# Optimization experiments

Measured on AMD Instinct MI355X. Metric: run time of the kernel, lower is better.

Reference implementation:

```python
import jax, jax.numpy as jnp
import numpy as np

D_MODEL = 1024
N_HEADS = 16
HEAD_DIM = D_MODEL // N_HEADS
B, T = 4, 2048
EPS = 1e-5


def _layernorm(x, w, b):
    mu = jnp.mean(x, axis=-1, keepdims=True)
    var = jnp.mean(jnp.square(x - mu), axis=-1, keepdims=True)
    return (x - mu) * jax.lax.rsqrt(var + EPS) * w + b


def _heads(x, w, b):
    # x: [B,T,D]; w stored [in,out] so y = x @ w + b (== torch Linear)
    y = x @ w + b
    return y.reshape(B, T, N_HEADS, HEAD_DIM).transpose(0, 2, 1, 3)  # [B,H,T,hd]


def _attention(q, k, v):
    scores = jnp.einsum('bhqd,bhkd->bhqk', q, k) / np.sqrt(HEAD_DIM).astype(np.float32)
    attn = jax.nn.softmax(scores, axis=-1)  # dropout is identity in eval mode
    o = jnp.einsum('bhqk,bhkd->bhqd', attn, v)
    return o.transpose(0, 2, 1, 3).reshape(B, T, D_MODEL)


def setup_inputs() -> dict:
    key = jax.random.key(0)
    ks = jax.random.split(key, 16)
    s = 1.0 / np.sqrt(D_MODEL)
    def lin(k, din, dout):
        kw, kb = jax.random.split(k)
        return (jax.random.uniform(kw, (din, dout), jnp.float32, -s, s),
                jax.random.uniform(kb, (dout,), jnp.float32, -s, s))
    inp = {}
    inp['temporal_tokens'] = jax.random.normal(ks[0], (B, T, D_MODEL), jnp.float32)
    inp['feature_tokens'] = jax.random.normal(ks[1], (B, T, D_MODEL), jnp.float32)
    names = ['qt', 'kf', 'vf', 'qf', 'kt', 'vt', 'ot', 'of']
    for i, n in enumerate(names):
        w, b = lin(ks[2 + i], D_MODEL, D_MODEL)
        inp[n + '_w'], inp[n + '_b'] = w, b
    inp['fus1_w'], inp['fus1_b'] = lin(ks[10], 2 * D_MODEL, D_MODEL)
    inp['fus2_w'], inp['fus2_b'] = lin(ks[11], D_MODEL, D_MODEL)
    for n in ['ln_fus', 'ln_t', 'ln_f']:
        inp[n + '_w'] = jnp.ones((D_MODEL,), jnp.float32)
        inp[n + '_b'] = jnp.zeros((D_MODEL,), jnp.float32)
    return inp


def reference(temporal_tokens, feature_tokens,
              qt_w, qt_b, kf_w, kf_b, vf_w, vf_b,
              qf_w, qf_b, kt_w, kt_b, vt_w, vt_b,
              ot_w, ot_b, of_w, of_b,
              fus1_w, fus1_b, fus2_w, fus2_b,
              ln_fus_w, ln_fus_b, ln_t_w, ln_t_b, ln_f_w, ln_f_b):
    # temporal -> feature cross attention
    Qt = _heads(temporal_tokens, qt_w, qt_b)
    Kf = _heads(feature_tokens, kf_w, kf_b)
    Vf = _heads(feature_tokens, vf_w, vf_b)
    attn_t = _attention(Qt, Kf, Vf) @ ot_w + ot_b
    fused_t = _layernorm(temporal_tokens + attn_t, ln_t_w, ln_t_b)
    # feature -> temporal cross attention
    Qf = _heads(feature_tokens, qf_w, qf_b)
    Kt = _heads(temporal_tokens, kt_w, kt_b)
    Vt = _heads(temporal_tokens, vt_w, vt_b)
    attn_f = _attention(Qf, Kt, Vt) @ of_w + of_b
    fused_f = _layernorm(feature_tokens + attn_f, ln_f_w, ln_f_b)
    # fusion MLP
    combined = jnp.concatenate([fused_t, fused_f], axis=-1)  # [B,T,2D]
    h = jax.nn.gelu(combined @ fus1_w + fus1_b, approximate=False)
    fused = _layernorm(h @ fus2_w + fus2_b, ln_fus_w, ln_fus_b)
    return fused
```

## Files before the change

### kernel.cpp

```cpp
#include <hip/hip_runtime.h>
#include <math.h>

typedef __attribute__((ext_vector_type(8))) short short8;
typedef __attribute__((ext_vector_type(4))) short short4v;
typedef __attribute__((ext_vector_type(4))) float floatx4;
typedef __attribute__((ext_vector_type(16))) float floatx16;

#define GLOBAL_AS __attribute__((address_space(1)))
#define LDS_AS __attribute__((address_space(3)))

__device__ __forceinline__ float bf2f(unsigned short u) {
    unsigned int x = ((unsigned int)u) << 16;
    return __builtin_bit_cast(float, x);
}
__device__ __forceinline__ unsigned short f2bf(float f) {
    unsigned int u = __builtin_bit_cast(unsigned int, f);
    u += 0x7fffu + ((u >> 16) & 1u);
    return (unsigned short)(u >> 16);
}

struct WX {
    const float* src[10];
    unsigned long long dst[10];
    int r64[10];
    int cum[11];
};

__global__ __launch_bounds__(256) void prep_kernel(
    WX P, unsigned short* __restrict__ base,
    const float* __restrict__ ta, const float* __restrict__ tb,
    unsigned short* __restrict__ oa, unsigned short* __restrict__ ob)
{
    __shared__ unsigned short T[64][72];
    const int bx = blockIdx.x;
    if (bx >= P.cum[10]) {
        const int cb = bx - P.cum[10];
        const float* in = cb < 1024 ? ta : tb;
        unsigned short* out = cb < 1024 ? oa : ob;
        const size_t b0 = (size_t)(cb & 1023) * 8192;
        #pragma unroll
        for (int j = 0; j < 8; ++j) {
            const size_t i = b0 + (size_t)j * 1024 + threadIdx.x * 4;
            float4 f = *(const float4*)(in + i);
            unsigned short o[4] = {f2bf(f.x), f2bf(f.y), f2bf(f.z), f2bf(f.w)};
            *(uint2*)(out + i) = *(const uint2*)o;
        }
        return;
    }
    int w = 0;
    #pragma unroll
    for (int i = 0; i < 10; ++i) if (bx >= P.cum[i + 1]) w = i + 1;
    const int tix = bx - P.cum[w];
    const int R = P.r64[w] * 64;
    const int r0 = (tix >> 4) * 64, c0 = (tix & 15) * 64;
    const float* in = P.src[w];
    unsigned short* out = base + P.dst[w];
    const int t = threadIdx.x;
    {
        const int r = t >> 2, cc = (t & 3) * 16;
        const float* p = in + (size_t)(r0 + r) * 1024 + c0 + cc;
        #pragma unroll
        for (int j = 0; j < 16; j += 4) {
            float4 f = *(const float4*)(p + j);
            T[cc + j + 0][r] = f2bf(f.x);
            T[cc + j + 1][r] = f2bf(f.y);
            T[cc + j + 2][r] = f2bf(f.z);
            T[cc + j + 3][r] = f2bf(f.w);
        }
    }
    __syncthreads();
    {
        const int c = t >> 2, rr = (t & 3) * 16;
        unsigned short* q = out + (size_t)(c0 + c) * R + r0 + rr;
        *(uint4*)(q)     = *(const uint4*)(&T[c][rr]);
        *(uint4*)(q + 8) = *(const uint4*)(&T[c][rr + 8]);
    }
}

#define GEMM_CORE(A_, B_, Kdim)                                               \
    const int tid = threadIdx.x;                                              \
    const int wave = tid >> 6, lane = tid & 63;                               \
    const int l32 = lane & 31, hi = lane >> 5;                                \
    const int wm = (wave & 1) * 64, wn = (wave >> 1) * 64;                    \
    const int srow8 = lane >> 3, c8 = lane & 7;                               \
    const int scol = (c8 ^ srow8) * 8;                                        \
    floatx16 acc[2][2];                                                       \
    _Pragma("unroll")                                                         \
    for (int i = 0; i < 2; ++i)                                               \
        _Pragma("unroll")                                                     \
        for (int j = 0; j < 2; ++j)                                           \
            _Pragma("unroll")                                                 \
            for (int r = 0; r < 16; ++r) acc[i][j][r] = 0.f;                  \
    const unsigned short* pa[4];                                              \
    const unsigned short* pb[4];                                              \
    _Pragma("unroll")                                                         \
    for (int i = 0; i < 4; ++i) {                                             \
        pa[i] = (A_) + (size_t)(bm + i * 32 + wave * 8 + srow8) * (Kdim) + scol; \
        pb[i] = (B_) + (size_t)(bn + i * 32 + wave * 8 + srow8) * (Kdim) + scol; \
    }                                                                         \
    int aoff[2][4], boff[2][4];                                               \
    _Pragma("unroll")                                                         \
    for (int f = 0; f < 2; ++f)                                               \
        _Pragma("unroll")                                                     \
        for (int s = 0; s < 4; ++s) {                                         \
            const int cg = ((s * 2 + hi) ^ (l32 & 7)) * 8;                    \
            aoff[f][s] = (wm + f * 32 + l32) * 64 + cg;                       \
            boff[f][s] = (wn + f * 32 + l32) * 64 + cg;                       \
        }                                                                     \
    for (int k0 = 0; k0 < (Kdim); k0 += 64) {                                 \
        _Pragma("unroll")                                                     \
        for (int i = 0; i < 4; ++i) {                                         \
            __builtin_amdgcn_global_load_lds((const GLOBAL_AS void*)(pa[i] + k0), \
                (LDS_AS void*)(As + i * 2048 + wave * 512), 16, 0, 0);        \
            __builtin_amdgcn_global_load_lds((const GLOBAL_AS void*)(pb[i] + k0), \
                (LDS_AS void*)(Bs + i * 2048 + wave * 512), 16, 0, 0);        \
        }                                                                     \
        __syncthreads();                                                      \
        _Pragma("unroll")                                                     \
        for (int s = 0; s < 4; ++s) {                                         \
            short8 af[2], bf[2];                                              \
            _Pragma("unroll")                                                 \
            for (int f = 0; f < 2; ++f) {                                     \
                af[f] = *(const short8*)&As[aoff[f][s]];                      \
                bf[f] = *(const short8*)&Bs[boff[f][s]];                      \
            }                                                                 \
            _Pragma("unroll")                                                 \
            for (int mi = 0; mi < 2; ++mi)                                    \
                _Pragma("unroll")                                             \
                for (int ni = 0; ni < 2; ++ni)                                \
                    acc[mi][ni] = __builtin_amdgcn_mfma_f32_32x32x16_bf16(    \
                        bf[ni], af[mi], acc[mi][ni], 0, 0, 0);                \
        }                                                                     \
        __syncthreads();                                                      \
    }

template <int MODE>
__global__ __launch_bounds__(256) void gemm_kernel(
    const unsigned short* __restrict__ A,
    const unsigned short* __restrict__ Wt,
    const float* __restrict__ bias,
    unsigned short* __restrict__ C,
    int N, int K)
{
    __shared__ unsigned short As[128 * 64];
    __shared__ unsigned short Bs[128 * 64];
    const int bm = blockIdx.x * 128, bn = blockIdx.y * 128;
    GEMM_CORE(A, Wt, K)

    #pragma unroll
    for (int mi = 0; mi < 2; ++mi) {
        const int m = bm + wm + mi * 32 + l32;
        #pragma unroll
        for (int ni = 0; ni < 2; ++ni) {
            #pragma unroll
            for (int rg = 0; rg < 4; ++rg) {
                const int n0 = bn + wn + ni * 32 + rg * 8 + hi * 4;
                float4 bv = *(const float4*)&bias[n0];
                float v[4];
                #pragma unroll
                for (int r = 0; r < 4; ++r)
                    v[r] = acc[mi][ni][rg * 4 + r] + ((const float*)&bv)[r];
                if (MODE == 2) {
                    #pragma unroll
                    for (int r = 0; r < 4; ++r)
                        v[r] = 0.5f * v[r] * (1.0f + erff(v[r] * 0.70710678118f));
                }
                unsigned short o[4] = {f2bf(v[0]), f2bf(v[1]), f2bf(v[2]), f2bf(v[3])};
                *(uint2*)&C[(size_t)m * N + n0] = *(const uint2*)o;
            }
        }
    }
}

__global__ __launch_bounds__(256) void gemm_out_kernel(
    const unsigned short* __restrict__ A0, const unsigned short* __restrict__ W0,
    const float* __restrict__ bi0, const float* __restrict__ r0, unsigned short* __restrict__ C0,
    const unsigned short* __restrict__ A1, const unsigned short* __restrict__ W1,
    const float* __restrict__ bi1, const float* __restrict__ r1, unsigned short* __restrict__ C1)
{
    __shared__ unsigned short As[128 * 64];
    __shared__ unsigned short Bs[128 * 64];
    const int s1 = blockIdx.y >> 3;
    const unsigned short* A = s1 ? A1 : A0;
    const unsigned short* Wt = s1 ? W1 : W0;
    const float* bias = s1 ? bi1 : bi0;
    const float* resid = s1 ? r1 : r0;
    unsigned short* C = s1 ? C1 : C0;
    const int bm = blockIdx.x * 128, bn = (blockIdx.y & 7) * 128;
    GEMM_CORE(A, Wt, 1024)

    #pragma unroll
    for (int mi = 0; mi < 2; ++mi) {
        const int m = bm + wm + mi * 32 + l32;
        #pragma unroll
        for (int ni = 0; ni < 2; ++ni) {
            #pragma unroll
            for (int rg = 0; rg < 4; ++rg) {
                const int n0 = bn + wn + ni * 32 + rg * 8 + hi * 4;
                float4 bv = *(const float4*)&bias[n0];
                float4 rv = *(const float4*)&resid[(size_t)m * 1024 + n0];
                float v[4];
                v[0] = acc[mi][ni][rg * 4 + 0] + bv.x + rv.x;
                v[1] = acc[mi][ni][rg * 4 + 1] + bv.y + rv.y;
                v[2] = acc[mi][ni][rg * 4 + 2] + bv.z + rv.z;
                v[3] = acc[mi][ni][rg * 4 + 3] + bv.w + rv.w;
                unsigned short o[4] = {f2bf(v[0]), f2bf(v[1]), f2bf(v[2]), f2bf(v[3])};
                *(uint2*)&C[(size_t)m * 1024 + n0] = *(const uint2*)o;
            }
        }
    }
}

__global__ __launch_bounds__(256) void gemm_qkv_kernel(
    const unsigned short* __restrict__ At, const unsigned short* __restrict__ Wt3t,
    const float* __restrict__ tb0, const float* __restrict__ tb1, const float* __restrict__ tb2,
    unsigned short* __restrict__ to0, unsigned short* __restrict__ to1, unsigned short* __restrict__ to2,
    const unsigned short* __restrict__ Af, const unsigned short* __restrict__ Wt3f,
    const float* __restrict__ fb0, const float* __restrict__ fb1, const float* __restrict__ fb2,
    unsigned short* __restrict__ fo0, unsigned short* __restrict__ fo1, unsigned short* __restrict__ fo2,
    float scale0)
{
    __shared__ unsigned short As[128 * 64];
    __shared__ unsigned short Bs[128 * 64];
    const int str = blockIdx.y >= 24;
    const unsigned short* A = str ? Af : At;
    const unsigned short* Wt = str ? Wt3f : Wt3t;
    const int byy = str ? (blockIdx.y - 24) : blockIdx.y;
    const int buf = byy >> 3;
    const int bn = byy * 128;
    const int cn = (byy & 7) * 128;
    const float* bias = str ? (buf == 0 ? fb0 : (buf == 1 ? fb1 : fb2))
                            : (buf == 0 ? tb0 : (buf == 1 ? tb1 : tb2));
    unsigned short* C = str ? (buf == 0 ? fo0 : (buf == 1 ? fo1 : fo2))
                            : (buf == 0 ? to0 : (buf == 1 ? to1 : to2));
    const float scale = buf == 0 ? scale0 : 1.0f;
    const int bm = blockIdx.x * 128;
    GEMM_CORE(A, Wt, 1024)

    #pragma unroll
    for (int mi = 0; mi < 2; ++mi) {
        const int m = bm + wm + mi * 32 + l32;
        #pragma unroll
        for (int ni = 0; ni < 2; ++ni) {
            #pragma unroll
            for (int rg = 0; rg < 4; ++rg) {
                const int n0 = cn + wn + ni * 32 + rg * 8 + hi * 4;
                float4 bv = *(const float4*)&bias[n0];
                unsigned short o[4];
                #pragma unroll
                for (int r = 0; r < 4; ++r)
                    o[r] = f2bf((acc[mi][ni][rg * 4 + r] + ((const float*)&bv)[r]) * scale);
                if (buf == 2) {
                    const int b = m >> 11, t = m & 2047;
                    const int h = n0 >> 6, d0 = n0 & 63;
                    const int tsw = t ^ ((d0 & 8) ? 4 : 0);
                    unsigned short* vb = C + ((size_t)(b * 16 + h) * 64) * 2048 + tsw;
                    #pragma unroll
                    for (int r = 0; r < 4; ++r) vb[(size_t)(d0 + r) * 2048] = o[r];
                } else {
                    *(uint2*)&C[(size_t)m * 1024 + n0] = *(const uint2*)o;
                }
            }
        }
    }
}

__global__ __launch_bounds__(256) void flash_kernel(
    const unsigned short* __restrict__ Q0, const unsigned short* __restrict__ K0,
    const unsigned short* __restrict__ V0, unsigned short* __restrict__ O0,
    const unsigned short* __restrict__ Q1, const unsigned short* __restrict__ K1,
    const unsigned short* __restrict__ V1, unsigned short* __restrict__ O1)
{
    __shared__ unsigned short Ks[64 * 64];
    __shared__ unsigned short Vs[64 * 64];

    const int bid = blockIdx.x;
    const int p = (bid & 7) * 16 + (bid >> 7);
    const int qt = (bid >> 3) & 15;
    const int s1 = p >= 64;
    const int rem = p & 63;
    const int b = rem >> 4, h = rem & 15;
    const unsigned short* Q = s1 ? Q1 : Q0;
    const unsigned short* Kmat = s1 ? K1 : K0;
    const unsigned short* Vtp = s1 ? V1 : V0;
    unsigned short* O = s1 ? O1 : O0;
    const int q0 = qt * 128;

    const int tid = threadIdx.x;
    const int wave = tid >> 6, lane = tid & 63;
    const int quad = lane >> 4, l16 = lane & 15;

    const unsigned short* qp = Q + (size_t)(b * 2048 + q0 + wave * 32 + l16) * 1024 + h * 64;
    short8 qf[2][2];
    qf[0][0] = *(const short8*)(qp + quad * 8);
    qf[0][1] = *(const short8*)(qp + 32 + quad * 8);
    qf[1][0] = *(const short8*)(qp + 16 * 1024 + quad * 8);
    qf[1][1] = *(const short8*)(qp + 16 * 1024 + 32 + quad * 8);

    const int srow8 = lane >> 3;
    const int c8 = lane & 7;
    const int rit0 = wave * 16 + srow8;
    const int rit1 = rit0 + 8;
    const int col0 = (c8 ^ (rit0 & 7)) * 8;
    const int col1 = (c8 ^ (rit1 & 7)) * 8;
    const unsigned short* kbase = Kmat + (size_t)b * 2048 * 1024 + h * 64;
    const unsigned short* vbase = Vtp + (size_t)(b * 16 + h) * 64 * 2048;
    unsigned short* lk0 = Ks + (wave * 16) * 64;
    unsigned short* lk1 = lk0 + 8 * 64;
    unsigned short* lv0 = Vs + (wave * 16) * 64;
    unsigned short* lv1 = lv0 + 8 * 64;

    int koff[4][2];
    #pragma unroll
    for (int nt = 0; nt < 4; ++nt)
        #pragma unroll
        for (int hh = 0; hh < 2; ++hh)
            koff[nt][hh] = (nt * 16 + l16) * 64 + (((hh * 4 + quad) ^ (l16 & 7)) * 8);
    int voff[4][4];
    #pragma unroll
    for (int dt = 0; dt < 4; ++dt)
        #pragma unroll
        for (int nt = 0; nt < 4; ++nt)
            voff[dt][nt] = (dt * 16 + l16) * 64 +
                           (((nt * 2 + (quad >> 1)) ^ (l16 & 7)) * 8) +
                           (((quad & 1) ^ (l16 >> 3)) * 4);

    floatx4 oa[2][4], la[2];
    #pragma unroll
    for (int qg = 0; qg < 2; ++qg) {
        la[qg] = (floatx4){0.f, 0.f, 0.f, 0.f};
        #pragma unroll
        for (int dt = 0; dt < 4; ++dt) oa[qg][dt] = (floatx4){0.f, 0.f, 0.f, 0.f};
    }
    const short4v vone = {(short)0x3F80, (short)0x3F80, (short)0x3F80, (short)0x3F80};

    for (int kt = 0; kt < 32; ++kt) {
        const unsigned short* kg0 = kbase + (size_t)(kt * 64 + rit0) * 1024 + col0;
        const unsigned short* kg1 = kbase + (size_t)(kt * 64 + rit1) * 1024 + col1;
        const unsigned short* vg0 = vbase + (size_t)rit0 * 2048 + kt * 64 + col0;
        const unsigned short* vg1 = vbase + (size_t)rit1 * 2048 + kt * 64 + col1;
        __builtin_amdgcn_global_load_lds((const GLOBAL_AS void*)kg0, (LDS_AS void*)lk0, 16, 0, 0);
        __builtin_amdgcn_global_load_lds((const GLOBAL_AS void*)kg1, (LDS_AS void*)lk1, 16, 0, 0);
        __builtin_amdgcn_global_load_lds((const GLOBAL_AS void*)vg0, (LDS_AS void*)lv0, 16, 0, 0);
        __builtin_amdgcn_global_load_lds((const GLOBAL_AS void*)vg1, (LDS_AS void*)lv1, 16, 0, 0);
        __syncthreads();

        short4v pf[2][4];
        #pragma unroll
        for (int nt = 0; nt < 4; ++nt) {
            short8 k0 = *(const short8*)&Ks[koff[nt][0]];
            short8 k1 = *(const short8*)&Ks[koff[nt][1]];
            #pragma unroll
            for (int qg = 0; qg < 2; ++qg) {
                floatx4 s = (floatx4){0.f, 0.f, 0.f, 0.f};
                s = __builtin_amdgcn_mfma_f32_16x16x32_bf16(k0, qf[qg][0], s, 0, 0, 0);
                s = __builtin_amdgcn_mfma_f32_16x16x32_bf16(k1, qf[qg][1], s, 0, 0, 0);
                float p0 = __builtin_amdgcn_exp2f(s[0]);
                float p1 = __builtin_amdgcn_exp2f(s[1]);
                float p2 = __builtin_amdgcn_exp2f(s[2]);
                float p3 = __builtin_amdgcn_exp2f(s[3]);
                union { unsigned u[2]; short4v s4; } pk;
                asm("v_cvt_pk_bf16_f32 %0, %1, %2"
                    : "=v"(pk.u[0]) : "v"(p0), "v"(p1));
                asm("v_cvt_pk_bf16_f32 %0, %1, %2"
                    : "=v"(pk.u[1]) : "v"(p2), "v"(p3));
                pf[qg][nt] = pk.s4;
                la[qg] = __builtin_amdgcn_mfma_f32_16x16x16bf16_1k(vone, pf[qg][nt], la[qg], 0, 0, 0);
            }
        }
        #pragma unroll
        for (int dt = 0; dt < 4; ++dt)
            #pragma unroll
            for (int nt = 0; nt < 4; ++nt) {
                short4v vf = *(const short4v*)&Vs[voff[dt][nt]];
                oa[0][dt] = __builtin_amdgcn_mfma_f32_16x16x16bf16_1k(vf, pf[0][nt], oa[0][dt], 0, 0, 0);
                oa[1][dt] = __builtin_amdgcn_mfma_f32_16x16x16bf16_1k(vf, pf[1][nt], oa[1][dt], 0, 0, 0);
            }
        __syncthreads();
    }

    #pragma unroll
    for (int qg = 0; qg < 2; ++qg) {
        const float linv = 1.0f / la[qg][0];
        unsigned short* orow = O + (size_t)(b * 2048 + q0 + wave * 32 + qg * 16 + l16) * 1024 + h * 64;
        #pragma unroll
        for (int dt = 0; dt < 4; ++dt) {
            unsigned short ob[4];
            #pragma unroll
            for (int r = 0; r < 4; ++r) ob[r] = f2bf(oa[qg][dt][r] * linv);
            *(uint2*)(orow + dt * 16 + quad * 4) = *(const uint2*)ob;
        }
    }
}

__global__ __launch_bounds__(256) void ln2_kernel(
    const unsigned short* __restrict__ in0, const unsigned short* __restrict__ in1,
    unsigned short* __restrict__ out,
    const float* __restrict__ w0, const float* __restrict__ b0,
    const float* __restrict__ w1, const float* __restrict__ b1)
{
    __shared__ float red[8];
    const int sel = blockIdx.x >> 13;
    const int row = blockIdx.x & 8191;
    const unsigned short* in = sel ? in1 : in0;
    const float* w = sel ? w1 : w0;
    const float* bb = sel ? b1 : b0;
    const int tid = threadIdx.x;
    const int wave = tid >> 6, lane = tid & 63;
    uint2 raw = *(const uint2*)(in + (size_t)row * 1024 + tid * 4);
    float v[4];
    v[0] = bf2f((unsigned short)(raw.x & 0xffffu));
    v[1] = bf2f((unsigned short)(raw.x >> 16));
    v[2] = bf2f((unsigned short)(raw.y & 0xffffu));
    v[3] = bf2f((unsigned short)(raw.y >> 16));
    float s = v[0] + v[1] + v[2] + v[3];
    float sq = v[0] * v[0] + v[1] * v[1] + v[2] * v[2] + v[3] * v[3];
    #pragma unroll
    for (int m = 1; m < 64; m <<= 1) { s += __shfl_xor(s, m); sq += __shfl_xor(sq, m); }
    if (lane == 0) { red[wave] = s; red[4 + wave] = sq; }
    __syncthreads();
    s = red[0] + red[1] + red[2] + red[3];
    sq = red[4] + red[5] + red[6] + red[7];
    const float mu = s * (1.0f / 1024.0f);
    const float var = sq * (1.0f / 1024.0f) - mu * mu;
    const float rstd = rsqrtf(var + 1e-5f);
    unsigned short ob[4];
    #pragma unroll
    for (int j = 0; j < 4; ++j)
        ob[j] = f2bf((v[j] - mu) * rstd * w[tid * 4 + j] + bb[tid * 4 + j]);
    *(uint2*)(out + (size_t)row * 2048 + sel * 1024 + tid * 4) = *(uint2*)ob;
}

__global__ __launch_bounds__(256) void ln_final_kernel(
    const unsigned short* __restrict__ in, float* __restrict__ out,
    const float* __restrict__ w, const float* __restrict__ bias)
{
    __shared__ float red[8];
    const int row = blockIdx.x;
    const int tid = threadIdx.x;
    const int wave = tid >> 6, lane = tid & 63;
    uint2 raw = *(const uint2*)(in + (size_t)row * 1024 + tid * 4);
    float v[4];
    v[0] = bf2f((unsigned short)(raw.x & 0xffffu));
    v[1] = bf2f((unsigned short)(raw.x >> 16));
    v[2] = bf2f((unsigned short)(raw.y & 0xffffu));
    v[3] = bf2f((unsigned short)(raw.y >> 16));
    float s = v[0] + v[1] + v[2] + v[3];
    float sq = v[0] * v[0] + v[1] * v[1] + v[2] * v[2] + v[3] * v[3];
    #pragma unroll
    for (int m = 1; m < 64; m <<= 1) { s += __shfl_xor(s, m); sq += __shfl_xor(sq, m); }
    if (lane == 0) { red[wave] = s; red[4 + wave] = sq; }
    __syncthreads();
    s = red[0] + red[1] + red[2] + red[3];
    sq = red[4] + red[5] + red[6] + red[7];
    const float mu = s * (1.0f / 1024.0f);
    const float var = sq * (1.0f / 1024.0f) - mu * mu;
    const float rstd = rsqrtf(var + 1e-5f);
    float o[4];
    #pragma unroll
    for (int j = 0; j < 4; ++j)
        o[j] = (v[j] - mu) * rstd * w[tid * 4 + j] + bias[tid * 4 + j];
    *(float4*)(out + (size_t)row * 1024 + tid * 4) = (float4){o[0], o[1], o[2], o[3]};
}

extern "C" void kernel_launch(void* const* d_in, const int* in_sizes, int n_in,
                              void* d_out, int out_size, void* d_ws, size_t ws_size,
                              hipStream_t stream)
{
    (void)in_sizes; (void)n_in; (void)out_size; (void)ws_size;
    const float* temporal = (const float*)d_in[0];
    const float* feature  = (const float*)d_in[1];
    const float* qt_w = (const float*)d_in[2];
    const float* qt_b = (const float*)d_in[3];
    const float* kf_w = (const float*)d_in[4];
    const float* kf_b = (const float*)d_in[5];
    const float* vf_w = (const float*)d_in[6];
    const float* vf_b = (const float*)d_in[7];
    const float* qf_w = (const float*)d_in[8];
    const float* qf_b = (const float*)d_in[9];
    const float* kt_w = (const float*)d_in[10];
    const float* kt_b = (const float*)d_in[11];
    const float* vt_w = (const float*)d_in[12];
    const float* vt_b = (const float*)d_in[13];
    const float* ot_w = (const float*)d_in[14];
    const float* ot_b = (const float*)d_in[15];
    const float* of_w = (const float*)d_in[16];
    const float* of_b = (const float*)d_in[17];
    const float* fus1_w = (const float*)d_in[18];
    const float* fus1_b = (const float*)d_in[19];
    const float* fus2_w = (const float*)d_in[20];
    const float* fus2_b = (const float*)d_in[21];
    const float* ln_fus_w = (const float*)d_in[22];
    const float* ln_fus_b = (const float*)d_in[23];
    const float* ln_t_w = (const float*)d_in[24];
    const float* ln_t_b = (const float*)d_in[25];
    const float* ln_f_w = (const float*)d_in[26];
    const float* ln_f_b = (const float*)d_in[27];

    unsigned short* p = (unsigned short*)d_ws;
    const size_t EW = 1024ull * 1024;
    const size_t ET = 8192ull * 1024;
    unsigned short* WT3t = p;
    unsigned short* WT3f = p + 3 * EW;
    unsigned short* WTot = p + 6 * EW;
    unsigned short* WTof = p + 7 * EW;
    unsigned short* WTf1 = p + 8 * EW;
    unsigned short* WTf2 = p + 10 * EW;
    size_t off = 11 * EW;
    unsigned short* Tb = p + off; off += ET;
    unsigned short* Fb = p + off; off += ET;
    unsigned short* Qt = p + off; off += ET;
    unsigned short* Kt = p + off; off += ET;
    unsigned short* Vt = p + off; off += ET;
    unsigned short* Qf = p + off; off += ET;
    unsigned short* Kf = p + off; off += ET;
    unsigned short* Vf = p + off; off += ET;
    unsigned short* VfT = p + off; off += ET;
    unsigned short* VtT = p + off; off += ET;
    unsigned short* attnT = p + off; off += ET;
    unsigned short* attnF = p + off; off += ET;
    unsigned short* yT = Qt;
    unsigned short* yF = Qf;
    unsigned short* comb = Kt;
    unsigned short* hbuf = Kf;
    unsigned short* y2 = Vf;
    (void)Vt;

    const float SC = 0.125f * 1.4426950408889634f;

    {
        WX P;
        const float* srcs[10] = {qt_w, kt_w, vt_w, qf_w, kf_w, vf_w,
                                 ot_w, of_w, fus1_w, fus2_w};
        unsigned long long dsts[10] = {
            0, EW, 2 * EW,
            3 * EW, 4 * EW, 5 * EW,
            6 * EW, 7 * EW, 8 * EW, 10 * EW};
        int cum = 0;
        P.cum[0] = 0;
        for (int i = 0; i < 10; ++i) {
            P.src[i] = srcs[i];
            P.dst[i] = dsts[i];
            P.r64[i] = (i == 8) ? 32 : 16;
            cum += P.r64[i] * 16;
            P.cum[i + 1] = cum;
        }
        prep_kernel<<<cum + 2048, 256, 0, stream>>>(P, p, temporal, feature, Tb, Fb);
    }

    const dim3 gb(256);
    gemm_qkv_kernel<<<dim3(64, 48), gb, 0, stream>>>(
        Tb, WT3t, qt_b, kt_b, vt_b, Qt, Kt, VtT,
        Fb, WT3f, qf_b, kf_b, vf_b, Qf, Kf, VfT, SC);
    flash_kernel<<<2048, gb, 0, stream>>>(
        Qt, Kf, VfT, attnT, Qf, Kt, VtT, attnF);
    gemm_out_kernel<<<dim3(64, 16), gb, 0, stream>>>(
        attnT, WTot, ot_b, temporal, yT,
        attnF, WTof, of_b, feature,  yF);
    ln2_kernel<<<16384, gb, 0, stream>>>(yT, yF, comb, ln_t_w, ln_t_b, ln_f_w, ln_f_b);
    gemm_kernel<2><<<dim3(64, 8), gb, 0, stream>>>(comb, WTf1, fus1_b, hbuf, 1024, 2048);
    gemm_kernel<0><<<dim3(64, 8), gb, 0, stream>>>(hbuf, WTf2, fus2_b, y2, 1024, 1024);
    ln_final_kernel<<<8192, gb, 0, stream>>>(y2, (float*)d_out, ln_fus_w, ln_fus_b);
}
```

Before: 676.1 us.

## Rewrite GEMM core as 256x256 tiles with double-buffered LDS pipeline

Replaces the 128x128 single-buffer GEMM core with a 256x256 tile computed by 8 waves using 16x16x32 MFMAs. Global-to-LDS loads are double-buffered and interleaved with the MFMA phases, using explicit vmcnt waits, barriers and setprio. All four GEMM kernels and their launch grids are adapted. The aim is to hide load latency and get more reuse per tile. The cost is a 128KB LDS footprint and heavy register use, and the grids shrink to as few as 128 blocks for the fusion GEMMs, which may underfill the GPU.

```diff
diff --git a/kernel.cpp b/kernel.cpp
--- a/kernel.cpp
+++ b/kernel.cpp
@@ -77,141 +77,200 @@
     }
 }
 
-#define GEMM_CORE(A_, B_, Kdim)                                               \
+#define G256_DECL(A_, B_, Kdim)                                               \
     const int tid = threadIdx.x;                                              \
     const int wave = tid >> 6, lane = tid & 63;                               \
-    const int l32 = lane & 31, hi = lane >> 5;                                \
-    const int wm = (wave & 1) * 64, wn = (wave >> 1) * 64;                    \
-    const int srow8 = lane >> 3, c8 = lane & 7;                               \
-    const int scol = (c8 ^ srow8) * 8;                                        \
-    floatx16 acc[2][2];                                                       \
+    const int quad = lane >> 4, l16 = lane & 15;                              \
+    const int wr = wave >> 2, wc = wave & 3;                                  \
+    const int lrow8 = lane >> 3, lc8 = lane & 7;                              \
+    floatx4 acc[8][4];                                                        \
     _Pragma("unroll")                                                         \
-    for (int i = 0; i < 2; ++i)                                               \
+    for (int i = 0; i < 8; ++i)                                               \
         _Pragma("unroll")                                                     \
-        for (int j = 0; j < 2; ++j)                                           \
+        for (int j = 0; j < 4; ++j) acc[i][j] = (floatx4){0.f, 0.f, 0.f, 0.f}; \
+    const unsigned short* sA[4];                                              \
+    const unsigned short* sB[4];                                              \
+    int ldst[4];                                                              \
+    _Pragma("unroll")                                                         \
+    for (int h = 0; h < 2; ++h)                                               \
+        _Pragma("unroll")                                                     \
+        for (int j = 0; j < 2; ++j) {                                         \
+            const int r0 = h * 128 + j * 64 + wave * 8;                       \
+            const int r = r0 + lrow8;                                         \
+            const int cg = lc8 ^ (r & 7);                                     \
+            sA[h * 2 + j] = (A_) + (size_t)(bm + r) * (Kdim) + cg * 8;        \
+            sB[h * 2 + j] = (B_) + (size_t)(bn + r) * (Kdim) + cg * 8;        \
+            ldst[h * 2 + j] = r0 * 64;                                        \
+        }
+
+#define G256_STG_A(s_) __builtin_amdgcn_global_load_lds(                      \
+    (const GLOBAL_AS void*)(sA[s_] + ko), (LDS_AS void*)(L + cb + ldst[s_]), 16, 0, 0)
+#define G256_STG_B(s_) __builtin_amdgcn_global_load_lds(                      \
+    (const GLOBAL_AS void*)(sB[s_] + ko), (LDS_AS void*)(L + cb + 16384 + ldst[s_]), 16, 0, 0)
+
+#define G256_LDA(mh_)                                                         \
+    _Pragma("unroll")                                                         \
+    for (int mi = 0; mi < 4; ++mi) {                                          \
+        const int r = (mh_) * 128 + wr * 64 + mi * 16 + l16;                  \
+        _Pragma("unroll")                                                     \
+        for (int kk = 0; kk < 2; ++kk)                                        \
+            afc[mi][kk] = *(const short8*)&L[cb + r * 64 +                    \
+                (((kk * 4 + quad) ^ (r & 7)) * 8)];                           \
+    }
+#define G256_LDB(nh_)                                                         \
+    _Pragma("unroll")                                                         \
+    for (int nj = 0; nj < 2; ++nj) {                                          \
+        const int r = (nh_) * 128 + wc * 32 + nj * 16 + l16;                  \
+        _Pragma("unroll")                                                     \
+        for (int kk = 0; kk < 2; ++kk)                                        \
+            bfr[(nh_) * 2 + nj][kk] = *(const short8*)&L[cb + 16384 + r * 64 +\
+                (((kk * 4 + quad) ^ (r & 7)) * 8)];                           \
+    }
+
+#define G256_FENCE() do {                                                     \
+    asm volatile("s_waitcnt lgkmcnt(0)" ::: "memory");                        \
+    __builtin_amdgcn_sched_barrier(0);                                        \
+    __builtin_amdgcn_s_barrier(); } while (0)
+
+#define G256_MM(mh_, nb_) do {                                                \
+    __builtin_amdgcn_s_setprio(1);                                            \
+    _Pragma("unroll")                                                         \
+    for (int mi = 0; mi < 4; ++mi)                                            \
+        _Pragma("unroll")                                                     \
+        for (int nj = 0; nj < 2; ++nj)                                        \
             _Pragma("unroll")                                                 \
-            for (int r = 0; r < 16; ++r) acc[i][j][r] = 0.f;                  \
-    const unsigned short* pa[4];                                              \
-    const unsigned short* pb[4];                                              \
-    _Pragma("unroll")                                                         \
-    for (int i = 0; i < 4; ++i) {                                             \
-        pa[i] = (A_) + (size_t)(bm + i * 32 + wave * 8 + srow8) * (Kdim) + scol; \
-        pb[i] = (B_) + (size_t)(bn + i * 32 + wave * 8 + srow8) * (Kdim) + scol; \
-    }                                                                         \
-    int aoff[2][4], boff[2][4];                                               \
-    _Pragma("unroll")                                                         \
-    for (int f = 0; f < 2; ++f)                                               \
+            for (int kk = 0; kk < 2; ++kk)                                    \
+                acc[(mh_) * 4 + mi][(nb_) + nj] =                             \
+                    __builtin_amdgcn_mfma_f32_16x16x32_bf16(                  \
+                        bfr[(nb_) + nj][kk], afc[mi][kk],                     \
+                        acc[(mh_) * 4 + mi][(nb_) + nj], 0, 0, 0);            \
+    __builtin_amdgcn_s_setprio(0); } while (0)
+
+#define G256_CORE(A_, B_, Kdim)                                               \
+    G256_DECL(A_, B_, Kdim)                                                   \
+    {                       \
         _Pragma("unroll")                                                     \
         for (int s = 0; s < 4; ++s) {                                         \
-            const int cg = ((s * 2 + hi) ^ (l32 & 7)) * 8;                    \
-            aoff[f][s] = (wm + f * 32 + l32) * 64 + cg;                       \
-            boff[f][s] = (wn + f * 32 + l32) * 64 + cg;                       \
+            __builtin_amdgcn_global_load_lds((const GLOBAL_AS void*)(sA[s]),  \
+                (LDS_AS void*)(L + ldst[s]), 16, 0, 0);                       \
+            __builtin_amdgcn_global_load_lds((const GLOBAL_AS void*)(sB[s]),  \
+                (LDS_AS void*)(L + 16384 + ldst[s]), 16, 0, 0);               \
         }                                                                     \
-    for (int k0 = 0; k0 < (Kdim); k0 += 64) {                                 \
-        _Pragma("unroll")                                                     \
-        for (int i = 0; i < 4; ++i) {                                         \
-            __builtin_amdgcn_global_load_lds((const GLOBAL_AS void*)(pa[i] + k0), \
-                (LDS_AS void*)(As + i * 2048 + wave * 512), 16, 0, 0);        \
-            __builtin_amdgcn_global_load_lds((const GLOBAL_AS void*)(pb[i] + k0), \
-                (LDS_AS void*)(Bs + i * 2048 + wave * 512), 16, 0, 0);        \
-        }                                                                     \
-        __syncthreads();                                                      \
         _Pragma("unroll")                                                     \
         for (int s = 0; s < 4; ++s) {                                         \
-            short8 af[2], bf[2];                                              \
-            _Pragma("unroll")                                                 \
-            for (int f = 0; f < 2; ++f) {                                     \
-                af[f] = *(const short8*)&As[aoff[f][s]];                      \
-                bf[f] = *(const short8*)&Bs[boff[f][s]];                      \
-            }                                                                 \
-            _Pragma("unroll")                                                 \
-            for (int mi = 0; mi < 2; ++mi)                                    \
-                _Pragma("unroll")                                             \
-                for (int ni = 0; ni < 2; ++ni)                                \
-                    acc[mi][ni] = __builtin_amdgcn_mfma_f32_32x32x16_bf16(    \
-                        bf[ni], af[mi], acc[mi][ni], 0, 0, 0);                \
+            __builtin_amdgcn_global_load_lds((const GLOBAL_AS void*)(sA[s] + 64), \
+                (LDS_AS void*)(L + 32768 + ldst[s]), 16, 0, 0);               \
+            __builtin_amdgcn_global_load_lds((const GLOBAL_AS void*)(sB[s] + 64), \
+                (LDS_AS void*)(L + 32768 + 16384 + ldst[s]), 16, 0, 0);       \
         }                                                                     \
-        __syncthreads();                                                      \
-    }
+        asm volatile("s_waitcnt vmcnt(8)" ::: "memory");                      \
+        __builtin_amdgcn_s_barrier();                                         \
+    }                                                                         \
+    short8 afc[4][2];                                                         \
+    short8 bfr[4][2];                                                         \
+    const int NT = (Kdim) >> 6;                                               \
+    for (int t = 0; t < NT; ++t) {                                            \
+        const int cb = (t & 1) << 15;                                         \
+        const int ko = (t + 2) << 6;                                          \
+        const bool stg = (t < NT - 2);                                        \
+                                                                      \
+        G256_LDA(0)                                                           \
+        G256_LDB(0)                                                           \
+        G256_FENCE();                                                         \
+        G256_MM(0, 0);                                                        \
+                                                                      \
+        G256_LDB(1)                                                           \
+        if (stg) { G256_STG_A(0); G256_STG_A(1); G256_STG_B(0); G256_STG_B(1); } \
+        G256_FENCE();                                                         \
+        G256_MM(0, 2);                                                        \
+                                                                      \
+        G256_LDA(1)                                                           \
+        if (stg) { G256_STG_B(2); G256_STG_B(3); }                            \
+        G256_FENCE();                                                         \
+        G256_MM(1, 2);                                                        \
+                                                                      \
+        if (stg) {                                                            \
+            G256_STG_A(2); G256_STG_A(3);                                     \
+            asm volatile("s_waitcnt vmcnt(8)" ::: "memory");                  \
+        } else {                                                              \
+            asm volatile("s_waitcnt vmcnt(0)" ::: "memory");                  \
+        }                                                                     \
+        __builtin_amdgcn_sched_barrier(0);                                    \
+        __builtin_amdgcn_s_barrier();                                         \
+        G256_MM(1, 0);                                                        \
+    }
+
 
 template <int MODE>
-__global__ __launch_bounds__(256) void gemm_kernel(
+__global__ __launch_bounds__(512, 2) void gemm_kernel(
     const unsigned short* __restrict__ A,
     const unsigned short* __restrict__ Wt,
     const float* __restrict__ bias,
     unsigned short* __restrict__ C,
     int N, int K)
 {
-    __shared__ unsigned short As[128 * 64];
-    __shared__ unsigned short Bs[128 * 64];
-    const int bm = blockIdx.x * 128, bn = blockIdx.y * 128;
-    GEMM_CORE(A, Wt, K)
-
-    #pragma unroll
-    for (int mi = 0; mi < 2; ++mi) {
-        const int m = bm + wm + mi * 32 + l32;
-        #pragma unroll
-        for (int ni = 0; ni < 2; ++ni) {
+    __shared__ unsigned short L[65536];
+    const int bm = blockIdx.x * 256, bn = blockIdx.y * 256;
+    G256_CORE(A, Wt, K)
+
+    #pragma unroll
+    for (int i = 0; i < 8; ++i) {
+        const int m = bm + (i >> 2) * 128 + wr * 64 + (i & 3) * 16 + l16;
+        #pragma unroll
+        for (int j = 0; j < 4; ++j) {
+            const int n0 = bn + (j >> 1) * 128 + wc * 32 + (j & 1) * 16 + quad * 4;
+            float4 bv = *(const float4*)&bias[n0];
+            float v[4];
             #pragma unroll
-            for (int rg = 0; rg < 4; ++rg) {
-                const int n0 = bn + wn + ni * 32 + rg * 8 + hi * 4;
-                float4 bv = *(const float4*)&bias[n0];
-                float v[4];
+            for (int r = 0; r < 4; ++r)
+                v[r] = acc[i][j][r] + ((const float*)&bv)[r];
+            if (MODE == 2) {
                 #pragma unroll
                 for (int r = 0; r < 4; ++r)
-                    v[r] = acc[mi][ni][rg * 4 + r] + ((const float*)&bv)[r];
-                if (MODE == 2) {
-                    #pragma unroll
-                    for (int r = 0; r < 4; ++r)
-                        v[r] = 0.5f * v[r] * (1.0f + erff(v[r] * 0.70710678118f));
-                }
-                unsigned short o[4] = {f2bf(v[0]), f2bf(v[1]), f2bf(v[2]), f2bf(v[3])};
-                *(uint2*)&C[(size_t)m * N + n0] = *(const uint2*)o;
+                    v[r] = 0.5f * v[r] * (1.0f + erff(v[r] * 0.70710678118f));
             }
-        }
-    }
-}
-
-__global__ __launch_bounds__(256) void gemm_out_kernel(
+            unsigned short o[4] = {f2bf(v[0]), f2bf(v[1]), f2bf(v[2]), f2bf(v[3])};
+            *(uint2*)&C[(size_t)m * N + n0] = *(const uint2*)o;
+        }
+    }
+}
+
+__global__ __launch_bounds__(512, 2) void gemm_out_kernel(
     const unsigned short* __restrict__ A0, const unsigned short* __restrict__ W0,
     const float* __restrict__ bi0, const float* __restrict__ r0, unsigned short* __restrict__ C0,
     const unsigned short* __restrict__ A1, const unsigned short* __restrict__ W1,
     const float* __restrict__ bi1, const float* __restrict__ r1, unsigned short* __restrict__ C1)
 {
-    __shared__ unsigned short As[128 * 64];
-    __shared__ unsigned short Bs[128 * 64];
-    const int s1 = blockIdx.y >> 3;
+    __shared__ unsigned short L[65536];
+    const int s1 = blockIdx.y >> 2;
     const unsigned short* A = s1 ? A1 : A0;
     const unsigned short* Wt = s1 ? W1 : W0;
     const float* bias = s1 ? bi1 : bi0;
     const float* resid = s1 ? r1 : r0;
     unsigned short* C = s1 ? C1 : C0;
-    const int bm = blockIdx.x * 128, bn = (blockIdx.y & 7) * 128;
-    GEMM_CORE(A, Wt, 1024)
-
-    #pragma unroll
-    for (int mi = 0; mi < 2; ++mi) {
-        const int m = bm + wm + mi * 32 + l32;
-        #pragma unroll
-        for (int ni = 0; ni < 2; ++ni) {
-            #pragma unroll
-            for (int rg = 0; rg < 4; ++rg) {
-                const int n0 = bn + wn + ni * 32 + rg * 8 + hi * 4;
-                float4 bv = *(const float4*)&bias[n0];
-                float4 rv = *(const float4*)&resid[(size_t)m * 1024 + n0];
-                float v[4];
-                v[0] = acc[mi][ni][rg * 4 + 0] + bv.x + rv.x;
-                v[1] = acc[mi][ni][rg * 4 + 1] + bv.y + rv.y;
-                v[2] = acc[mi][ni][rg * 4 + 2] + bv.z + rv.z;
-                v[3] = acc[mi][ni][rg * 4 + 3] + bv.w + rv.w;
-                unsigned short o[4] = {f2bf(v[0]), f2bf(v[1]), f2bf(v[2]), f2bf(v[3])};
-                *(uint2*)&C[(size_t)m * 1024 + n0] = *(const uint2*)o;
-            }
-        }
-    }
-}
-
-__global__ __launch_bounds__(256) void gemm_qkv_kernel(
+    const int bm = blockIdx.x * 256, bn = (blockIdx.y & 3) * 256;
+    G256_CORE(A, Wt, 1024)
+
+    #pragma unroll
+    for (int i = 0; i < 8; ++i) {
+        const int m = bm + (i >> 2) * 128 + wr * 64 + (i & 3) * 16 + l16;
+        #pragma unroll
+        for (int j = 0; j < 4; ++j) {
+            const int n0 = bn + (j >> 1) * 128 + wc * 32 + (j & 1) * 16 + quad * 4;
+            float4 bv = *(const float4*)&bias[n0];
+            float4 rv = *(const float4*)&resid[(size_t)m * 1024 + n0];
+            float v[4];
+            v[0] = acc[i][j][0] + bv.x + rv.x;
+            v[1] = acc[i][j][1] + bv.y + rv.y;
+            v[2] = acc[i][j][2] + bv.z + rv.z;
+            v[3] = acc[i][j][3] + bv.w + rv.w;
+            unsigned short o[4] = {f2bf(v[0]), f2bf(v[1]), f2bf(v[2]), f2bf(v[3])};
+            *(uint2*)&C[(size_t)m * 1024 + n0] = *(const uint2*)o;
+        }
+    }
+}
+
+__global__ __launch_bounds__(512, 2) void gemm_qkv_kernel(
     const unsigned short* __restrict__ At, const unsigned short* __restrict__ Wt3t,
     const float* __restrict__ tb0, const float* __restrict__ tb1, const float* __restrict__ tb2,
     unsigned short* __restrict__ to0, unsigned short* __restrict__ to1, unsigned short* __restrict__ to2,
@@ -220,46 +279,42 @@
     unsigned short* __restrict__ fo0, unsigned short* __restrict__ fo1, unsigned short* __restrict__ fo2,
     float scale0)
 {
-    __shared__ unsigned short As[128 * 64];
-    __shared__ unsigned short Bs[128 * 64];
-    const int str = blockIdx.y >= 24;
+    __shared__ unsigned short L[65536];
+    const int str = blockIdx.y >= 12;
     const unsigned short* A = str ? Af : At;
     const unsigned short* Wt = str ? Wt3f : Wt3t;
-    const int byy = str ? (blockIdx.y - 24) : blockIdx.y;
-    const int buf = byy >> 3;
-    const int bn = byy * 128;
-    const int cn = (byy & 7) * 128;
+    const int byy = str ? (blockIdx.y - 12) : blockIdx.y;
+    const int buf = byy >> 2;
+    const int bn = byy * 256;
+    const int cn = (byy & 3) * 256;
     const float* bias = str ? (buf == 0 ? fb0 : (buf == 1 ? fb1 : fb2))
                             : (buf == 0 ? tb0 : (buf == 1 ? tb1 : tb2));
     unsigned short* C = str ? (buf == 0 ? fo0 : (buf == 1 ? fo1 : fo2))
                             : (buf == 0 ? to0 : (buf == 1 ? to1 : to2));
     const float scale = buf == 0 ? scale0 : 1.0f;
-    const int bm = blockIdx.x * 128;
-    GEMM_CORE(A, Wt, 1024)
-
-    #pragma unroll
-    for (int mi = 0; mi < 2; ++mi) {
-        const int m = bm + wm + mi * 32 + l32;
-        #pragma unroll
-        for (int ni = 0; ni < 2; ++ni) {
+    const int bm = blockIdx.x * 256;
+    G256_CORE(A, Wt, 1024)
+
+    #pragma unroll
+    for (int i = 0; i < 8; ++i) {
+        const int m = bm + (i >> 2) * 128 + wr * 64 + (i & 3) * 16 + l16;
+        #pragma unroll
+        for (int j = 0; j < 4; ++j) {
+            const int n0 = cn + (j >> 1) * 128 + wc * 32 + (j & 1) * 16 + quad * 4;
+            float4 bv = *(const float4*)&bias[n0];
+            unsigned short o[4];
             #pragma unroll
-            for (int rg = 0; rg < 4; ++rg) {
-                const int n0 = cn + wn + ni * 32 + rg * 8 + hi * 4;
-                float4 bv = *(const float4*)&bias[n0];
-                unsigned short o[4];
+            for (int r = 0; r < 4; ++r)
+                o[r] = f2bf((acc[i][j][r] + ((const float*)&bv)[r]) * scale);
+            if (buf == 2) {
+                const int b = m >> 11, tk = m & 2047;
+                const int h = n0 >> 6, d0 = n0 & 63;
+                const int tsw = tk ^ ((d0 & 8) ? 4 : 0);
+                unsigned short* vb = C + ((size_t)(b * 16 + h) * 64) * 2048 + tsw;
                 #pragma unroll
-                for (int r = 0; r < 4; ++r)
-                    o[r] = f2bf((acc[mi][ni][rg * 4 + r] + ((const float*)&bv)[r]) * scale);
-                if (buf == 2) {
-                    const int b = m >> 11, t = m & 2047;
-                    const int h = n0 >> 6, d0 = n0 & 63;
-                    const int tsw = t ^ ((d0 & 8) ? 4 : 0);
-                    unsigned short* vb = C + ((size_t)(b * 16 + h) * 64) * 2048 + tsw;
-                    #pragma unroll
-                    for (int r = 0; r < 4; ++r) vb[(size_t)(d0 + r) * 2048] = o[r];
-                } else {
-                    *(uint2*)&C[(size_t)m * 1024 + n0] = *(const uint2*)o;
-                }
+                for (int r = 0; r < 4; ++r) vb[(size_t)(d0 + r) * 2048] = o[r];
+            } else {
+                *(uint2*)&C[(size_t)m * 1024 + n0] = *(const uint2*)o;
             }
         }
     }
@@ -548,17 +603,17 @@
         prep_kernel<<<cum + 2048, 256, 0, stream>>>(P, p, temporal, feature, Tb, Fb);
     }
 
-    const dim3 gb(256);
-    gemm_qkv_kernel<<<dim3(64, 48), gb, 0, stream>>>(
+    const dim3 gb5(512);
+    gemm_qkv_kernel<<<dim3(32, 24), gb5, 0, stream>>>(
         Tb, WT3t, qt_b, kt_b, vt_b, Qt, Kt, VtT,
         Fb, WT3f, qf_b, kf_b, vf_b, Qf, Kf, VfT, SC);
-    flash_kernel<<<2048, gb, 0, stream>>>(
+    flash_kernel<<<2048, dim3(256), 0, stream>>>(
         Qt, Kf, VfT, attnT, Qf, Kt, VtT, attnF);
-    gemm_out_kernel<<<dim3(64, 16), gb, 0, stream>>>(
+    gemm_out_kernel<<<dim3(32, 8), gb5, 0, stream>>>(
         attnT, WTot, ot_b, temporal, yT,
         attnF, WTof, of_b, feature,  yF);
-    ln2_kernel<<<16384, gb, 0, stream>>>(yT, yF, comb, ln_t_w, ln_t_b, ln_f_w, ln_f_b);
-    gemm_kernel<2><<<dim3(64, 8), gb, 0, stream>>>(comb, WTf1, fus1_b, hbuf, 1024, 2048);
-    gemm_kernel<0><<<dim3(64, 8), gb, 0, stream>>>(hbuf, WTf2, fus2_b, y2, 1024, 1024);
-    ln_final_kernel<<<8192, gb, 0, stream>>>(y2, (float*)d_out, ln_fus_w, ln_fus_b);
-}
+    ln2_kernel<<<16384, dim3(256), 0, stream>>>(yT, yF, comb, ln_t_w, ln_t_b, ln_f_w, ln_f_b);
+    gemm_kernel<2><<<dim3(32, 4), gb5, 0, stream>>>(comb, WTf1, fus1_b, hbuf, 1024, 2048);
+    gemm_kernel<0><<<dim3(32, 4), gb5, 0, stream>>>(hbuf, WTf2, fus2_b, y2, 1024, 1024);
+    ln_final_kernel<<<8192, dim3(256), 0, stream>>>(y2, (float*)d_out, ln_fus_w, ln_fus_b);
+}
```

Result: faster. 660.3 us (-2.3%).
